# Performance work log

Hardware: AMD Instinct MI355X
Metric: run time of the kernel (lower is better)

Reference implementation:

```python
import jax, jax.numpy as jnp
import numpy as np

N_NODES = 100000
N_EDGES = 1600000
IN_C, HID_C, OUT_C = 128, 128, 64


def gcn_conv(x, src, dst, W, b, num_nodes):
    # PyG GCNConv: add self-loops, symmetric normalization, linear transform,
    # aggregate source features into targets.
    h = x @ W  # [N, C_out]
    loop = jnp.arange(num_nodes, dtype=src.dtype)
    s = jnp.concatenate([src, loop])
    d = jnp.concatenate([dst, loop])
    deg = jax.ops.segment_sum(jnp.ones_like(d, dtype=h.dtype), d, num_segments=num_nodes)
    inv_sqrt = jnp.where(deg > 0, jax.lax.rsqrt(deg), 0.0)
    norm = inv_sqrt[s] * inv_sqrt[d]  # [E+N]
    msgs = h[s] * norm[:, None]  # gather + scale
    out = jax.ops.segment_sum(msgs, d, num_segments=num_nodes)  # scatter-add
    return out + b


def setup_inputs() -> dict:
    key = jax.random.key(0)
    k1, k2, k3, k4 = jax.random.split(key, 4)
    x = jax.random.normal(k1, (N_NODES, IN_C), dtype=jnp.float32)
    edge_index = jax.random.randint(k2, (2, N_EDGES), 0, N_NODES, dtype=jnp.int64)
    W1 = jax.random.normal(k3, (IN_C, HID_C), dtype=jnp.float32) * (1.0 / np.sqrt(IN_C))
    b1 = jnp.zeros((HID_C,), dtype=jnp.float32)
    W2 = jax.random.normal(k4, (HID_C, OUT_C), dtype=jnp.float32) * (1.0 / np.sqrt(HID_C))
    b2 = jnp.zeros((OUT_C,), dtype=jnp.float32)
    return {"x": x, "edge_index": edge_index, "W1": W1, "b1": b1, "W2": W2, "b2": b2}


def reference(x, edge_index, W1, b1, W2, b2):
    num_nodes = x.shape[0]
    src, dst = edge_index[0], edge_index[1]  # PyG flow: source -> target
    h = gcn_conv(x, src, dst, W1, b1, num_nodes)
    h = jax.nn.relu(h)  # dropout is identity in eval mode
    out = gcn_conv(h, src, dst, W2, b2, num_nodes)
    return out
```

## Files before the change

### kernel.cpp

```cpp
#include <hip/hip_runtime.h>

#define IN_C 128
#define HID_C 128
#define OUT_C 64

#define BSPAN 256
#define BCAP  5120
#define NBMAX 512
#define ACHUNK 4096

typedef unsigned int uint32;
typedef unsigned short ushort16;
typedef _Float16 f16;
typedef f16   f16x8 __attribute__((ext_vector_type(8)));
typedef float f32x4 __attribute__((ext_vector_type(4)));


__device__ __forceinline__ ushort16 f2bf(float f) {
    union { float f; uint32 u; } v; v.f = f;
    uint32 r = v.u + 0x7FFFu + ((v.u >> 16) & 1u);
    return (ushort16)(r >> 16);
}

__device__ __forceinline__ void unpack2(uint32 u, float& f0, float& f1) {
    union { uint32 x; float f; } a, b;
    a.x = u << 16;
    b.x = u & 0xFFFF0000u;
    f0 = a.f; f1 = b.f;
}

__device__ __forceinline__ void acc_row(uint4 r, float* acc) {
    float f0, f1;
    unpack2(r.x, f0, f1); acc[0] += f0; acc[1] += f1;
    unpack2(r.y, f0, f1); acc[2] += f0; acc[3] += f1;
    unpack2(r.z, f0, f1); acc[4] += f0; acc[5] += f1;
    unpack2(r.w, f0, f1); acc[6] += f0; acc[7] += f1;
}


__launch_bounds__(256)
__global__ void bin_edges_kernel(const int* __restrict__ src, const int* __restrict__ dst,
                                 int* __restrict__ bucketCur, uint32* __restrict__ binned,
                                 int E, int nbuck) {
    __shared__ int hist[NBMAX];
    __shared__ int base[NBMAX];
    const int tid = threadIdx.x;
    const int e0  = blockIdx.x * ACHUNK;

    for (int i = tid; i < NBMAX; i += 256) hist[i] = 0;
    __syncthreads();

    int d[16], s[16], rk[16];
#pragma unroll
    for (int j = 0; j < 16; j++) {
        int e = e0 + j * 256 + tid;
        if (e < E) {
            d[j] = dst[e];
            s[j] = src[e];
            rk[j] = atomicAdd(&hist[d[j] >> 8], 1);
        } else d[j] = -1;
    }
    __syncthreads();

    for (int b = tid; b < nbuck; b += 256) {
        int h = hist[b];
        base[b] = h ? atomicAdd(&bucketCur[b], h) : 0;
    }
    __syncthreads();

#pragma unroll
    for (int j = 0; j < 16; j++) {
        if (d[j] >= 0) {
            int b = d[j] >> 8;
            int pos = base[b] + rk[j];
            if (pos < BCAP)
                binned[(size_t)b * BCAP + pos] =
                    ((uint32)(d[j] & 255) << 17) | (uint32)s[j];
        }
    }
}


__launch_bounds__(256)
__global__ void bucket_csr_kernel(const uint32* __restrict__ binned,
                                  const int* __restrict__ bucketCur,
                                  int* __restrict__ csr_src, int* __restrict__ rowbeg,
                                  int* __restrict__ rowend, float* __restrict__ inv, int N) {
    constexpr int MAXIT = BCAP / 256;
    __shared__ int cnt[BSPAN];
    __shared__ int scn[BSPAN];
    __shared__ int excl[BSPAN];
    const int b   = blockIdx.x;
    const int tid = threadIdx.x;
    const int n0  = b * BSPAN;
    const int ne  = min(bucketCur[b], BCAP);
    const uint32* bp = binned + (size_t)b * BCAP;

    cnt[tid] = 0;
    __syncthreads();

    uint32 ebuf[MAXIT];
    int    rbuf[MAXIT];
    int nmine = 0;
    for (int i = tid; i < ne; i += 256) {
        uint32 e = bp[i];
        ebuf[nmine] = e;
        rbuf[nmine] = atomicAdd(&cnt[e >> 17], 1);
        nmine++;
    }
    __syncthreads();

    int v = cnt[tid];
    scn[tid] = v;
    __syncthreads();
    for (int off = 1; off < 256; off <<= 1) {
        int u = (tid >= off) ? scn[tid - off] : 0;
        __syncthreads();
        scn[tid] += u;
        __syncthreads();
    }
    int ex = scn[tid] - v;
    excl[tid] = ex;

    int n = n0 + tid;
    if (n < N) {
        int gb = b * BCAP + ex;
        rowbeg[n] = gb;
        rowend[n] = gb + v;
        inv[n] = rsqrtf((float)(v + 1));
    }
    __syncthreads();

    for (int j = 0; j < nmine; j++) {
        uint32 e = ebuf[j];
        csr_src[(size_t)b * BCAP + excl[e >> 17] + rbuf[j]] = (int)(e & 0x1FFFFu);
    }
}


template <int C>
__device__ __forceinline__ void wprep_one(const float* __restrict__ W, f16* __restrict__ Wf, int t) {
    constexpr int NCT = C / 16;
    int lane = t & 63;
    int ctkc = t >> 6;
    int ct = ctkc % NCT, kc = ctkc / NCT;
    int kbase = kc * 32 + (lane >> 4) * 8;
    int col   = ct * 16 + (lane & 15);
    f16 v[8];
#pragma unroll
    for (int j = 0; j < 8; j++) v[j] = (f16)W[(size_t)(kbase + j) * C + col];
    *(uint4*)(Wf + (size_t)t * 8) = *(const uint4*)v;
}

__global__ void wprep_both(const float* __restrict__ W1, f16* __restrict__ Wf1,
                           const float* __restrict__ W2, f16* __restrict__ Wf2,
                           int* __restrict__ bucketCur, int nbuck) {
    constexpr int T1 = 4 * (HID_C / 16) * 64;
    constexpr int T2 = 4 * (OUT_C / 16) * 64;
    int t = blockIdx.x * 256 + threadIdx.x;
    if (t < nbuck) bucketCur[t] = 0;
    if (t < T1)            wprep_one<HID_C>(W1, Wf1, t);
    else if (t < T1 + T2)  wprep_one<OUT_C>(W2, Wf2, t - T1);
}


template <int C>
__launch_bounds__(256)
__global__ void mfma_gemm(const float* __restrict__ X, const f16* __restrict__ Wf,
                          const float* __restrict__ inv, ushort16* __restrict__ outb, int N) {
    constexpr int NCT = C / 16;
    __shared__ __align__(16) f16 As[4 * 4 * 64 * 8];
    __shared__ __align__(16) f16 Bs[4 * NCT * 64 * 8];

    const int tid  = threadIdx.x;
    const int lane = tid & 63;
    const int w    = tid >> 6;
    const int row0 = blockIdx.x * 64;

    {
        constexpr int TOT = 4 * NCT * 64 * 8;
        const uint4* src = (const uint4*)Wf;
        uint4* dst = (uint4*)Bs;
#pragma unroll
        for (int i = 0; i < TOT / 8 / 256; i++)
            dst[tid + i * 256] = src[tid + i * 256];
    }

    {
        int r   = tid >> 2;
        int seg = tid & 3;
        int row = row0 + r;
        int ws_ = r >> 4;
        int r15 = r & 15;
#pragma unroll
        for (int i = 0; i < 8; i++) {
            int k = seg * 32 + i * 4;
            float4 v = make_float4(0.f, 0.f, 0.f, 0.f);
            if (row < N) v = *(const float4*)(X + (size_t)row * 128 + k);
            int q = (k >> 3) & 3, j0 = k & 7;
            f16 h[4] = {(f16)v.x, (f16)v.y, (f16)v.z, (f16)v.w};
            int slot = ((seg * 4 + ws_) * 64 + (q * 16 + r15)) * 8 + j0;
            *(uint2*)(As + slot) = *(const uint2*)h;
        }
    }
    __syncthreads();

    f32x4 acc[NCT];
#pragma unroll
    for (int c = 0; c < NCT; c++) acc[c] = (f32x4){0.f, 0.f, 0.f, 0.f};
#pragma unroll
    for (int kc = 0; kc < 4; kc++) {
        f16x8 a = *(const f16x8*)&As[((kc * 4 + w) * 64 + lane) * 8];
#pragma unroll
        for (int ct = 0; ct < NCT; ct++) {
            f16x8 b = *(const f16x8*)&Bs[((kc * NCT + ct) * 64 + lane) * 8];
            acc[ct] = __builtin_amdgcn_mfma_f32_16x16x32_f16(a, b, acc[ct], 0, 0, 0);
        }
    }

    __syncthreads();
    ushort16* Ds = (ushort16*)As;
    const int q = lane >> 4;
    float iv[4];
#pragma unroll
    for (int reg = 0; reg < 4; reg++) {
        int row = row0 + w * 16 + q * 4 + reg;
        iv[reg] = (row < N) ? inv[row] : 0.f;
    }
#pragma unroll
    for (int ct = 0; ct < NCT; ct++) {
#pragma unroll
        for (int reg = 0; reg < 4; reg++) {
            int r = w * 16 + q * 4 + reg;
            Ds[r * C + ct * 16 + (lane & 15)] = f2bf(acc[ct][reg] * iv[reg]);
        }
    }
    __syncthreads();
    {
        int r  = tid >> 2;
        int row = row0 + r;
        if (row < N) {
            constexpr int SPT = C / 4;
            int c0 = (tid & 3) * SPT;
            const uint4* s = (const uint4*)&Ds[r * C + c0];
            uint4* d = (uint4*)(outb + (size_t)row * C + c0);
#pragma unroll
            for (int i = 0; i < SPT / 8; i++) d[i] = s[i];
        }
    }
}


__launch_bounds__(256)
__global__ void fused_gather_gemm(const int* __restrict__ rowbeg, const int* __restrict__ rowend,
                                  const int* __restrict__ csr,
                                  const ushort16* __restrict__ hsb,
                                  const float* __restrict__ inv, const float* __restrict__ bias1,
                                  const f16* __restrict__ Wf2,
                                  ushort16* __restrict__ outb, int N) {
    constexpr int CIN = 128, COUT = 64, NCT = COUT / 16;
    __shared__ __align__(16) f16 As[4 * 4 * 64 * 8];
    __shared__ __align__(16) f16 Bs[4 * NCT * 64 * 8];

    const int tid  = threadIdx.x;
    const int lane = tid & 63;
    const int w    = tid >> 6;
    const int row0 = blockIdx.x * 64;

    {
        constexpr int TOT = 4 * NCT * 64 * 8;
        const uint4* s = (const uint4*)Wf2;
        uint4* d = (uint4*)Bs;
#pragma unroll
        for (int i = 0; i < TOT / 8 / 256; i++)
            d[tid + i * 256] = s[tid + i * 256];
    }

    {
        int r = tid >> 2;
        int q = tid & 3;
        int n = row0 + r;
        float acc[32];
#pragma unroll
        for (int j = 0; j < 32; j++) acc[j] = 0.f;

        if (n < N) {
            const ushort16* base = hsb + (size_t)n * CIN + q * 32;
            uint4 s0 = *(const uint4*)(base);
            uint4 s1 = *(const uint4*)(base + 8);
            uint4 s2 = *(const uint4*)(base + 16);
            uint4 s3 = *(const uint4*)(base + 24);
            acc_row(s0, acc); acc_row(s1, acc + 8); acc_row(s2, acc + 16); acc_row(s3, acc + 24);

            int beg = rowbeg[n], end = rowend[n];
            int i = beg;
            for (; i + 2 <= end; i += 2) {
                const ushort16* p0 = hsb + (size_t)csr[i]     * CIN + q * 32;
                const ushort16* p1 = hsb + (size_t)csr[i + 1] * CIN + q * 32;
                uint4 a0 = *(const uint4*)(p0);
                uint4 a1 = *(const uint4*)(p0 + 8);
                uint4 a2 = *(const uint4*)(p0 + 16);
                uint4 a3 = *(const uint4*)(p0 + 24);
                uint4 b0 = *(const uint4*)(p1);
                uint4 b1 = *(const uint4*)(p1 + 8);
                uint4 b2 = *(const uint4*)(p1 + 16);
                uint4 b3 = *(const uint4*)(p1 + 24);
                acc_row(a0, acc); acc_row(a1, acc + 8); acc_row(a2, acc + 16); acc_row(a3, acc + 24);
                acc_row(b0, acc); acc_row(b1, acc + 8); acc_row(b2, acc + 16); acc_row(b3, acc + 24);
            }
            if (i < end) {
                const ushort16* p0 = hsb + (size_t)csr[i] * CIN + q * 32;
                uint4 a0 = *(const uint4*)(p0);
                uint4 a1 = *(const uint4*)(p0 + 8);
                uint4 a2 = *(const uint4*)(p0 + 16);
                uint4 a3 = *(const uint4*)(p0 + 24);
                acc_row(a0, acc); acc_row(a1, acc + 8); acc_row(a2, acc + 16); acc_row(a3, acc + 24);
            }

            float iv = inv[n];
#pragma unroll
            for (int j = 0; j < 32; j++)
                acc[j] = fmaxf(fmaf(iv, acc[j], bias1[q * 32 + j]), 0.f);
        }

        int ws_ = r >> 4, r15 = r & 15;
#pragma unroll
        for (int i8 = 0; i8 < 4; i8++) {
            f16 h[8];
#pragma unroll
            for (int j = 0; j < 8; j++) h[j] = (f16)acc[i8 * 8 + j];
            int slot = ((q * 4 + ws_) * 64 + (i8 * 16 + r15)) * 8;
            *(uint4*)(As + slot) = *(const uint4*)h;
        }
    }
    __syncthreads();

    f32x4 acc2[NCT];
#pragma unroll
    for (int c = 0; c < NCT; c++) acc2[c] = (f32x4){0.f, 0.f, 0.f, 0.f};
#pragma unroll
    for (int kc = 0; kc < 4; kc++) {
        f16x8 a = *(const f16x8*)&As[((kc * 4 + w) * 64 + lane) * 8];
#pragma unroll
        for (int ct = 0; ct < NCT; ct++) {
            f16x8 b = *(const f16x8*)&Bs[((kc * NCT + ct) * 64 + lane) * 8];
            acc2[ct] = __builtin_amdgcn_mfma_f32_16x16x32_f16(a, b, acc2[ct], 0, 0, 0);
        }
    }

    __syncthreads();
    ushort16* Ds = (ushort16*)As;
    const int q2 = lane >> 4;
    float iv2[4];
#pragma unroll
    for (int reg = 0; reg < 4; reg++) {
        int row = row0 + w * 16 + q2 * 4 + reg;
        iv2[reg] = (row < N) ? inv[row] : 0.f;
    }
#pragma unroll
    for (int ct = 0; ct < NCT; ct++) {
#pragma unroll
        for (int reg = 0; reg < 4; reg++) {
            int r = w * 16 + q2 * 4 + reg;
            Ds[r * COUT + ct * 16 + (lane & 15)] = f2bf(acc2[ct][reg] * iv2[reg]);
        }
    }
    __syncthreads();
    {
        int r   = tid >> 2;
        int row = row0 + r;
        if (row < N) {
            constexpr int SPT = COUT / 4;
            int c0 = (tid & 3) * SPT;
            const uint4* s = (const uint4*)&Ds[r * COUT + c0];
            uint4* d = (uint4*)(outb + (size_t)row * COUT + c0);
#pragma unroll
            for (int i = 0; i < SPT / 8; i++) d[i] = s[i];
        }
    }
}


template <int C, bool RELU>
__launch_bounds__(256)
__global__ void gather_agg_bf16(const int* __restrict__ rowbeg, const int* __restrict__ rowend,
                                const int* __restrict__ csr_src,
                                const ushort16* __restrict__ hsb, const float* __restrict__ inv,
                                const float* __restrict__ b, float* __restrict__ out, int N) {
    constexpr int TPN = C / 8;
    constexpr int NPB = 256 / TPN;
    int n    = blockIdx.x * NPB + threadIdx.x / TPN;
    int lane = threadIdx.x % TPN;
    if (n >= N) return;
    int c8 = lane * 8;

    float acc[8];
    {
        uint4 raw = *(const uint4*)(hsb + (size_t)n * C + c8);
        unpack2(raw.x, acc[0], acc[1]);
        unpack2(raw.y, acc[2], acc[3]);
        unpack2(raw.z, acc[4], acc[5]);
        unpack2(raw.w, acc[6], acc[7]);
    }

    int beg = rowbeg[n];
    int end = rowend[n];
    int i = beg;
    for (; i + 4 <= end; i += 4) {
        int s0 = csr_src[i];
        int s1 = csr_src[i + 1];
        int s2 = csr_src[i + 2];
        int s3 = csr_src[i + 3];
        uint4 r0 = *(const uint4*)(hsb + (size_t)s0 * C + c8);
        uint4 r1 = *(const uint4*)(hsb + (size_t)s1 * C + c8);
        uint4 r2 = *(const uint4*)(hsb + (size_t)s2 * C + c8);
        uint4 r3 = *(const uint4*)(hsb + (size_t)s3 * C + c8);
        acc_row(r0, acc); acc_row(r1, acc); acc_row(r2, acc); acc_row(r3, acc);
    }
    for (; i < end; i++) {
        uint4 r0 = *(const uint4*)(hsb + (size_t)csr_src[i] * C + c8);
        acc_row(r0, acc);
    }

    float iv = inv[n];
    float4 b0 = *(const float4*)(b + c8);
    float4 b1 = *(const float4*)(b + c8 + 4);
    float r[8];
    r[0] = fmaf(iv, acc[0], b0.x); r[1] = fmaf(iv, acc[1], b0.y);
    r[2] = fmaf(iv, acc[2], b0.z); r[3] = fmaf(iv, acc[3], b0.w);
    r[4] = fmaf(iv, acc[4], b1.x); r[5] = fmaf(iv, acc[5], b1.y);
    r[6] = fmaf(iv, acc[6], b1.z); r[7] = fmaf(iv, acc[7], b1.w);
    if (RELU) {
#pragma unroll
        for (int j = 0; j < 8; j++) r[j] = fmaxf(r[j], 0.f);
    }
    float* po = out + (size_t)n * C + c8;
    *(float4*)(po)     = make_float4(r[0], r[1], r[2], r[3]);
    *(float4*)(po + 4) = make_float4(r[4], r[5], r[6], r[7]);
}

extern "C" void kernel_launch(void* const* d_in, const int* in_sizes, int n_in,
                              void* d_out, int out_size, void* d_ws, size_t ws_size,
                              hipStream_t stream) {
    const float* x  = (const float*)d_in[0];
    const int*   ei = (const int*)d_in[1];
    const float* W1 = (const float*)d_in[2];
    const float* b1 = (const float*)d_in[3];
    const float* W2 = (const float*)d_in[4];
    const float* b2 = (const float*)d_in[5];
    float* out = (float*)d_out;

    const int N = in_sizes[0] / IN_C;
    const int E = in_sizes[1] / 2;
    const int* src = ei;
    const int* dst = ei + E;
    const int nbuck = (N + BSPAN - 1) / BSPAN;

    char* ws = (char*)d_ws;
    auto align_up = [](size_t v) { return (v + 1023) & ~(size_t)1023; };
    size_t off = 0;
    int*      bucketCur = (int*)(ws + off);      off += align_up((size_t)nbuck * sizeof(int));
    float*    inv       = (float*)(ws + off);    off += align_up((size_t)N * sizeof(float));
    int*      rowbeg    = (int*)(ws + off);      off += align_up((size_t)N * sizeof(int));
    int*      rowend    = (int*)(ws + off);      off += align_up((size_t)N * sizeof(int));
    uint32*   binned    = (uint32*)(ws + off);   off += align_up((size_t)nbuck * BCAP * sizeof(uint32));
    int*      csrs      = (int*)(ws + off);      off += align_up((size_t)nbuck * BCAP * sizeof(int));
    f16*      Wf1       = (f16*)(ws + off);      off += align_up((size_t)4 * (HID_C/16) * 64 * 8 * sizeof(f16));
    f16*      Wf2       = (f16*)(ws + off);      off += align_up((size_t)4 * (OUT_C/16) * 64 * 8 * sizeof(f16));
    ushort16* hs1b      = (ushort16*)(ws + off); off += align_up((size_t)N * HID_C * sizeof(ushort16));
    ushort16* hs2b      = (ushort16*)(ws + off); off += align_up((size_t)N * OUT_C * sizeof(ushort16));

    wprep_both<<<(4 * (HID_C/16 + OUT_C/16) * 64 + 255) / 256, 256, 0, stream>>>(
        W1, Wf1, W2, Wf2, bucketCur, nbuck);
    bin_edges_kernel<<<(E + ACHUNK - 1) / ACHUNK, 256, 0, stream>>>(
        src, dst, bucketCur, binned, E, nbuck);
    bucket_csr_kernel<<<nbuck, 256, 0, stream>>>(
        binned, bucketCur, csrs, rowbeg, rowend, inv, N);

    mfma_gemm<HID_C><<<(N + 63) / 64, 256, 0, stream>>>(x, Wf1, inv, hs1b, N);

    fused_gather_gemm<<<(N + 63) / 64, 256, 0, stream>>>(
        rowbeg, rowend, csrs, hs1b, inv, b1, Wf2, hs2b, N);

    {
        constexpr int NPB = 256 / (OUT_C / 8);
        gather_agg_bf16<OUT_C, false><<<(N + NPB - 1) / NPB, 256, 0, stream>>>(
            rowbeg, rowend, csrs, hs2b, inv, b2, out, N);
    }
}
```

Before: 261.0 us.

## Split each node's edge gather across two thread halves in fused gather-GEMM

Doubles the fused gather+GEMM block to 512 threads so that each node row's neighbour list is split between two thread groups handling interleaved edges. The partial sums are combined with a cross-lane shuffle before bias/ReLU. The aim is more memory-level parallelism on the latency-bound neighbour gather. In exchange, half the waves sit idle during the MFMA stage, there is extra shuffle work, and the launch bounds request 8 waves per SIMD, which may force register spilling.

```diff
diff --git a/kernel.cpp b/kernel.cpp
--- a/kernel.cpp
+++ b/kernel.cpp
@@ -251,7 +251,7 @@
 }
 
 
-__launch_bounds__(256)
+__launch_bounds__(512, 8)
 __global__ void fused_gather_gemm(const int* __restrict__ rowbeg, const int* __restrict__ rowend,
                                   const int* __restrict__ csr,
                                   const ushort16* __restrict__ hsb,
@@ -268,35 +268,36 @@
     const int row0 = blockIdx.x * 64;
 
     {
-        constexpr int TOT = 4 * NCT * 64 * 8;
         const uint4* s = (const uint4*)Wf2;
         uint4* d = (uint4*)Bs;
-#pragma unroll
-        for (int i = 0; i < TOT / 8 / 256; i++)
-            d[tid + i * 256] = s[tid + i * 256];
-    }
-
-    {
-        int r = tid >> 2;
-        int q = tid & 3;
-        int n = row0 + r;
+        d[tid]       = s[tid];
+        d[tid + 512] = s[tid + 512];
+    }
+
+    {
+        const int r = tid >> 3;
+        const int h = (tid >> 2) & 1;
+        const int q = tid & 3;
+        const int n = row0 + r;
         float acc[32];
 #pragma unroll
         for (int j = 0; j < 32; j++) acc[j] = 0.f;
 
         if (n < N) {
-            const ushort16* base = hsb + (size_t)n * CIN + q * 32;
-            uint4 s0 = *(const uint4*)(base);
-            uint4 s1 = *(const uint4*)(base + 8);
-            uint4 s2 = *(const uint4*)(base + 16);
-            uint4 s3 = *(const uint4*)(base + 24);
-            acc_row(s0, acc); acc_row(s1, acc + 8); acc_row(s2, acc + 16); acc_row(s3, acc + 24);
-
-            int beg = rowbeg[n], end = rowend[n];
-            int i = beg;
-            for (; i + 2 <= end; i += 2) {
+            if (h == 0) {
+                const ushort16* base = hsb + (size_t)n * CIN + q * 32;
+                uint4 s0 = *(const uint4*)(base);
+                uint4 s1 = *(const uint4*)(base + 8);
+                uint4 s2 = *(const uint4*)(base + 16);
+                uint4 s3 = *(const uint4*)(base + 24);
+                acc_row(s0, acc); acc_row(s1, acc + 8);
+                acc_row(s2, acc + 16); acc_row(s3, acc + 24);
+            }
+            const int end = rowend[n];
+            int i = rowbeg[n] + h;
+            for (; i + 2 < end; i += 4) {
                 const ushort16* p0 = hsb + (size_t)csr[i]     * CIN + q * 32;
-                const ushort16* p1 = hsb + (size_t)csr[i + 1] * CIN + q * 32;
+                const ushort16* p1 = hsb + (size_t)csr[i + 2] * CIN + q * 32;
                 uint4 a0 = *(const uint4*)(p0);
                 uint4 a1 = *(const uint4*)(p0 + 8);
                 uint4 a2 = *(const uint4*)(p0 + 16);
@@ -316,21 +317,27 @@
                 uint4 a3 = *(const uint4*)(p0 + 24);
                 acc_row(a0, acc); acc_row(a1, acc + 8); acc_row(a2, acc + 16); acc_row(a3, acc + 24);
             }
-
+        }
+
+#pragma unroll
+        for (int j = 0; j < 32; j++) acc[j] += __shfl_xor(acc[j], 4, 64);
+
+        if (n < N) {
             float iv = inv[n];
 #pragma unroll
             for (int j = 0; j < 32; j++)
                 acc[j] = fmaxf(fmaf(iv, acc[j], bias1[q * 32 + j]), 0.f);
         }
 
-        int ws_ = r >> 4, r15 = r & 15;
-#pragma unroll
-        for (int i8 = 0; i8 < 4; i8++) {
-            f16 h[8];
-#pragma unroll
-            for (int j = 0; j < 8; j++) h[j] = (f16)acc[i8 * 8 + j];
+        const int ws_ = r >> 4, r15 = r & 15;
+#pragma unroll
+        for (int u = 0; u < 2; u++) {
+            const int i8 = h * 2 + u;
+            f16 hv[8];
+#pragma unroll
+            for (int j = 0; j < 8; j++) hv[j] = (f16)acc[i8 * 8 + j];
             int slot = ((q * 4 + ws_) * 64 + (i8 * 16 + r15)) * 8;
-            *(uint4*)(As + slot) = *(const uint4*)h;
+            *(uint4*)(As + slot) = *(const uint4*)hv;
         }
     }
     __syncthreads();
@@ -338,44 +345,44 @@
     f32x4 acc2[NCT];
 #pragma unroll
     for (int c = 0; c < NCT; c++) acc2[c] = (f32x4){0.f, 0.f, 0.f, 0.f};
-#pragma unroll
-    for (int kc = 0; kc < 4; kc++) {
-        f16x8 a = *(const f16x8*)&As[((kc * 4 + w) * 64 + lane) * 8];
+    if (w < 4) {
+#pragma unroll
+        for (int kc = 0; kc < 4; kc++) {
+            f16x8 a = *(const f16x8*)&As[((kc * 4 + w) * 64 + lane) * 8];
+#pragma unroll
+            for (int ct = 0; ct < NCT; ct++) {
+                f16x8 b = *(const f16x8*)&Bs[((kc * NCT + ct) * 64 + lane) * 8];
+                acc2[ct] = __builtin_amdgcn_mfma_f32_16x16x32_f16(a, b, acc2[ct], 0, 0, 0);
+            }
+        }
+    }
+
+    __syncthreads();
+    ushort16* Ds = (ushort16*)As;
+    if (w < 4) {
+        const int q2 = lane >> 4;
+        float iv2[4];
+#pragma unroll
+        for (int reg = 0; reg < 4; reg++) {
+            int row = row0 + w * 16 + q2 * 4 + reg;
+            iv2[reg] = (row < N) ? inv[row] : 0.f;
+        }
 #pragma unroll
         for (int ct = 0; ct < NCT; ct++) {
-            f16x8 b = *(const f16x8*)&Bs[((kc * NCT + ct) * 64 + lane) * 8];
-            acc2[ct] = __builtin_amdgcn_mfma_f32_16x16x32_f16(a, b, acc2[ct], 0, 0, 0);
-        }
-    }
-
-    __syncthreads();
-    ushort16* Ds = (ushort16*)As;
-    const int q2 = lane >> 4;
-    float iv2[4];
-#pragma unroll
-    for (int reg = 0; reg < 4; reg++) {
-        int row = row0 + w * 16 + q2 * 4 + reg;
-        iv2[reg] = (row < N) ? inv[row] : 0.f;
-    }
-#pragma unroll
-    for (int ct = 0; ct < NCT; ct++) {
-#pragma unroll
-        for (int reg = 0; reg < 4; reg++) {
-            int r = w * 16 + q2 * 4 + reg;
-            Ds[r * COUT + ct * 16 + (lane & 15)] = f2bf(acc2[ct][reg] * iv2[reg]);
-        }
-    }
-    __syncthreads();
-    {
-        int r   = tid >> 2;
-        int row = row0 + r;
+#pragma unroll
+            for (int reg = 0; reg < 4; reg++) {
+                int r = w * 16 + q2 * 4 + reg;
+                Ds[r * COUT + ct * 16 + (lane & 15)] = f2bf(acc2[ct][reg] * iv2[reg]);
+            }
+        }
+    }
+    __syncthreads();
+    {
+        const int r   = tid >> 3;
+        const int row = row0 + r;
         if (row < N) {
-            constexpr int SPT = COUT / 4;
-            int c0 = (tid & 3) * SPT;
-            const uint4* s = (const uint4*)&Ds[r * COUT + c0];
-            uint4* d = (uint4*)(outb + (size_t)row * COUT + c0);
-#pragma unroll
-            for (int i = 0; i < SPT / 8; i++) d[i] = s[i];
+            const int c0 = (tid & 7) * 8;
+            *(uint4*)(outb + (size_t)row * COUT + c0) = *(const uint4*)&Ds[r * COUT + c0];
         }
     }
 }
@@ -479,7 +486,7 @@
 
     mfma_gemm<HID_C><<<(N + 63) / 64, 256, 0, stream>>>(x, Wf1, inv, hs1b, N);
 
-    fused_gather_gemm<<<(N + 63) / 64, 256, 0, stream>>>(
+    fused_gather_gemm<<<(N + 63) / 64, 512, 0, stream>>>(
         rowbeg, rowend, csrs, hs1b, inv, b1, Wf2, hs2b, N);
 
     {
```

Measured after the change: 468.5 us. 1.8x slower.
